# Kernel optimization log

Hardware: AMD Instinct MI355X
Metric: run time of the kernel (lower is better)

The kernel has to match this reference:

```python
import jax, jax.numpy as jnp
import numpy as np

N_NODES = 8192


def _gcn_norm(edge_index, num_nodes):
    # PyG GCNConv default: add self-loops, symmetric normalization.
    src, dst = edge_index[0], edge_index[1]
    loop = jnp.arange(num_nodes, dtype=src.dtype)
    src = jnp.concatenate([src, loop])
    dst = jnp.concatenate([dst, loop])
    deg = jax.ops.segment_sum(jnp.ones_like(dst, dtype=jnp.float32), dst,
                              num_segments=num_nodes)
    dis = jnp.where(deg > 0, jax.lax.rsqrt(jnp.maximum(deg, 1.0)), 0.0)
    norm = dis[src] * dis[dst]  # [E + N]
    return src, dst, norm


def _gcn_conv(x, W, b, src, dst, norm, num_nodes):
    h = x @ W                           # [N, F_out] dense GEMM
    msg = h[src] * norm[:, None]        # gather + scale, [E+N, F_out]
    out = jax.ops.segment_sum(msg, dst, num_segments=num_nodes)  # scatter-add
    return out + b


def setup_inputs() -> dict:
    key = jax.random.key(0)
    ks = jax.random.split(key, 8)
    N, E, F_in, H1, H2, F_out = N_NODES, 65536, 512, 4096, 1024, 10
    x = jax.random.normal(ks[0], (N, F_in), dtype=jnp.float32)
    edge_index = jax.random.randint(ks[1], (2, E), 0, N, dtype=jnp.int64)
    # Glorot-ish scaled weights
    W1 = jax.random.normal(ks[2], (F_in, H1), dtype=jnp.float32) * (1.0 / np.sqrt(F_in))
    b1 = jnp.zeros((H1,), dtype=jnp.float32)
    W2 = jax.random.normal(ks[3], (H1, H2), dtype=jnp.float32) * (1.0 / np.sqrt(H1))
    b2 = jnp.zeros((H2,), dtype=jnp.float32)
    W3 = jax.random.normal(ks[4], (H2, F_out), dtype=jnp.float32) * (1.0 / np.sqrt(H2))
    b3 = jnp.zeros((F_out,), dtype=jnp.float32)
    return {"x": x, "W1": W1, "b1": b1, "W2": W2, "b2": b2,
            "W3": W3, "b3": b3, "edge_index": edge_index}


def reference(x, W1, b1, W2, b2, W3, b3, edge_index):
    N = N_NODES
    src, dst, norm = _gcn_norm(edge_index, N)
    h = _gcn_conv(x.astype(jnp.float32), W1, b1, src, dst, norm, N)
    h = jax.nn.relu(h)  # dropout is identity in eval mode
    h = _gcn_conv(h, W2, b2, src, dst, norm, N)
    h = jax.nn.relu(h)
    h = _gcn_conv(h, W3, b3, src, dst, norm, N)
    return jax.nn.log_softmax(h, axis=1)
```

## Files before the change

kernel.cpp:

```cpp
#include <hip/hip_runtime.h>
#include <math.h>

#define N_NODES 8192
#define N_EDGES 65536
#define F_IN    512
#define HID1    4096
#define HID2    1024
#define F_OUT   10
#define H3_STRIDE 12

typedef __bf16 bf16x8 __attribute__((ext_vector_type(8)));
typedef float floatx4 __attribute__((ext_vector_type(4)));

static __device__ __forceinline__ unsigned short f2bf(float f) {
    union { float f; unsigned u; } v; v.f = f;
    unsigned r = v.u + 0x7fffu + ((v.u >> 16) & 1u);
    return (unsigned short)(r >> 16);
}
static __device__ __forceinline__ float bf2f(unsigned short u) {
    union { unsigned u; float f; } v; v.u = ((unsigned)u) << 16;
    return v.f;
}

__global__ void deg_kernel(const int* __restrict__ ei, int* __restrict__ deg) {
    int e = blockIdx.x * blockDim.x + threadIdx.x;
    if (e < N_EDGES) atomicAdd(&deg[ei[N_EDGES + e]], 1);
}

__global__ __launch_bounds__(1024) void scan_kernel(const int* __restrict__ deg,
                                                    int* __restrict__ row_ptr,
                                                    int* __restrict__ cnt) {
    __shared__ int sums[1024];
    int t = threadIdx.x;
    int base = t * 8;
    int local[8];
    int run = 0;
#pragma unroll
    for (int i = 0; i < 8; i++) { local[i] = run; run += deg[base + i]; cnt[base + i] = 0; }
    sums[t] = run;
    __syncthreads();
    for (int off = 1; off < 1024; off <<= 1) {
        int val = (t >= off) ? sums[t - off] : 0;
        __syncthreads();
        sums[t] += val;
        __syncthreads();
    }
    int offset = (t == 0) ? 0 : sums[t - 1];
#pragma unroll
    for (int i = 0; i < 8; i++) row_ptr[base + i] = offset + local[i];
    if (t == 1023) row_ptr[N_NODES] = sums[1023];
}

__global__ void fill_kernel(const int* __restrict__ ei, const int* __restrict__ deg,
                            const int* __restrict__ row_ptr, int* __restrict__ cnt,
                            int* __restrict__ csr_src, float* __restrict__ csr_w) {
    int e = blockIdx.x * blockDim.x + threadIdx.x;
    if (e < N_EDGES) {
        int s = ei[e];
        int d = ei[N_EDGES + e];
        int slot = row_ptr[d] + atomicAdd(&cnt[d], 1);
        csr_src[slot] = s;
        csr_w[slot] = rsqrtf((float)((deg[s] + 1) * (deg[d] + 1)));
    }
}

static __device__ __forceinline__ void transpose_body(
        const float* __restrict__ W, unsigned short* __restrict__ Wt,
        int K, int N, int k0, int n0, int tid, float (*t)[33]) {
    int c = tid & 31, r8 = tid >> 5;
#pragma unroll
    for (int i = 0; i < 4; i++) {
        int r = r8 + i * 8;
        t[r][c] = W[(size_t)(k0 + r) * N + n0 + c];
    }
    __syncthreads();
#pragma unroll
    for (int i = 0; i < 4; i++) {
        int r = r8 + i * 8;
        Wt[(size_t)(n0 + r) * K + k0 + c] = f2bf(t[c][r]);
    }
}

__global__ __launch_bounds__(256) void prep_kernel(
        const float* __restrict__ x, unsigned short* __restrict__ xb,
        const float* __restrict__ W1, unsigned short* __restrict__ W1t,
        const float* __restrict__ W2, unsigned short* __restrict__ W2t) {
    __shared__ float t[32][33];
    int b = blockIdx.x, tid = threadIdx.x;
    if (b < 4096) {
        int i = b * 256 + tid;
        float4 a = ((const float4*)x)[i];
        ushort4 o;
        o.x = f2bf(a.x); o.y = f2bf(a.y); o.z = f2bf(a.z); o.w = f2bf(a.w);
        ((ushort4*)xb)[i] = o;
    } else if (b < 6144) {
        int bb = b - 4096;
        transpose_body(W1, W1t, F_IN, HID1, (bb >> 7) * 32, (bb & 127) * 32, tid, t);
    } else {
        int bb = b - 6144;
        transpose_body(W2, W2t, HID1, HID2, (bb >> 5) * 32, (bb & 31) * 32, tid, t);
    }
}

__global__ __launch_bounds__(256) void agg1_kernel(
        const unsigned short* __restrict__ xb, const int* __restrict__ row_ptr,
        const int* __restrict__ csr_src, const float* __restrict__ csr_w,
        const int* __restrict__ deg, unsigned short* __restrict__ out) {
    int v = blockIdx.x * 2 + (threadIdx.x >> 7);
    int t = threadIdx.x & 127;
    const ushort4* x4 = (const ushort4*)xb;
    float sw = 1.0f / (float)(deg[v] + 1);
    ushort4 a = x4[(size_t)v * 128 + t];
    float ax = sw * bf2f(a.x), ay = sw * bf2f(a.y), az = sw * bf2f(a.z), aw = sw * bf2f(a.w);
    int e = row_ptr[v], end = row_ptr[v + 1];
    for (; e + 2 <= end; e += 2) {
        int s0 = csr_src[e], s1 = csr_src[e + 1];
        float w0 = csr_w[e], w1 = csr_w[e + 1];
        ushort4 b0 = x4[(size_t)s0 * 128 + t];
        ushort4 b1 = x4[(size_t)s1 * 128 + t];
        ax += w0 * bf2f(b0.x) + w1 * bf2f(b1.x);
        ay += w0 * bf2f(b0.y) + w1 * bf2f(b1.y);
        az += w0 * bf2f(b0.z) + w1 * bf2f(b1.z);
        aw += w0 * bf2f(b0.w) + w1 * bf2f(b1.w);
    }
    if (e < end) {
        int s = csr_src[e];
        float w = csr_w[e];
        ushort4 b = x4[(size_t)s * 128 + t];
        ax += w * bf2f(b.x); ay += w * bf2f(b.y); az += w * bf2f(b.z); aw += w * bf2f(b.w);
    }
    ushort4 o;
    o.x = f2bf(ax); o.y = f2bf(ay); o.z = f2bf(az); o.w = f2bf(aw);
    ((ushort4*)out)[(size_t)v * 128 + t] = o;
}

__global__ __launch_bounds__(256) void agg2_kernel(
        const unsigned short* __restrict__ h, const int* __restrict__ row_ptr,
        const int* __restrict__ csr_src, const float* __restrict__ csr_w,
        const int* __restrict__ deg, const float* __restrict__ bias,
        unsigned short* __restrict__ out) {
    int v = blockIdx.x;
    int t = threadIdx.x;
    const ushort4* h4 = (const ushort4*)h;
    float sw = 1.0f / (float)(deg[v] + 1);
    ushort4 a = h4[(size_t)v * 256 + t];
    float ax = sw * bf2f(a.x), ay = sw * bf2f(a.y), az = sw * bf2f(a.z), aw = sw * bf2f(a.w);
    int e = row_ptr[v], end = row_ptr[v + 1];
    for (; e + 2 <= end; e += 2) {
        int s0 = csr_src[e], s1 = csr_src[e + 1];
        float w0 = csr_w[e], w1 = csr_w[e + 1];
        ushort4 b0 = h4[(size_t)s0 * 256 + t];
        ushort4 b1 = h4[(size_t)s1 * 256 + t];
        ax += w0 * bf2f(b0.x) + w1 * bf2f(b1.x);
        ay += w0 * bf2f(b0.y) + w1 * bf2f(b1.y);
        az += w0 * bf2f(b0.z) + w1 * bf2f(b1.z);
        aw += w0 * bf2f(b0.w) + w1 * bf2f(b1.w);
    }
    if (e < end) {
        int s = csr_src[e];
        float w = csr_w[e];
        ushort4 b = h4[(size_t)s * 256 + t];
        ax += w * bf2f(b.x); ay += w * bf2f(b.y); az += w * bf2f(b.z); aw += w * bf2f(b.w);
    }
    float4 bb = ((const float4*)bias)[t];
    ushort4 o;
    o.x = f2bf(fmaxf(ax + bb.x, 0.0f)); o.y = f2bf(fmaxf(ay + bb.y, 0.0f));
    o.z = f2bf(fmaxf(az + bb.z, 0.0f)); o.w = f2bf(fmaxf(aw + bb.w, 0.0f));
    ((ushort4*)out)[(size_t)v * 256 + t] = o;
}

template <bool OUT_BF16, bool BIAS, bool RELU>
__global__ __launch_bounds__(256) void gemm_mfma_kernel(
        const unsigned short* __restrict__ A,
        const unsigned short* __restrict__ Bt,
        const float* __restrict__ bias,
        void* __restrict__ C,
        int M, int N, int K) {
    __shared__ unsigned short As[128 * 64];
    __shared__ unsigned short Bs[128 * 64];
    int tid = threadIdx.x;
    int wave = tid >> 6, lane = tid & 63;
    int wm = wave >> 1, wn = wave & 1;
    int GN = N >> 7;
    int b = blockIdx.x;
    int ntile = (b >> 3) % GN;
    int mtile = ((b >> 3) / GN) * 8 + (b & 7);
    int m0 = mtile * 128, n0 = ntile * 128;
    int lrow = lane & 15, lquad = lane >> 4;

    floatx4 acc[4][4] = {};

    for (int k0 = 0; k0 < K; k0 += 64) {
#pragma unroll
        for (int j = 0; j < 4; j++) {
            int idx = j * 256 + tid;
            int r = idx >> 3;
            int kc = (idx & 7) ^ (r & 7);
            __builtin_amdgcn_global_load_lds(
                (const __attribute__((address_space(1))) void*)(A + (size_t)(m0 + r) * K + k0 + kc * 8),
                (__attribute__((address_space(3))) void*)(&As[idx * 8]), 16, 0, 0);
            __builtin_amdgcn_global_load_lds(
                (const __attribute__((address_space(1))) void*)(Bt + (size_t)(n0 + r) * K + k0 + kc * 8),
                (__attribute__((address_space(3))) void*)(&Bs[idx * 8]), 16, 0, 0);
        }
        __syncthreads();
#pragma unroll
        for (int kk = 0; kk < 2; kk++) {
            bf16x8 af[4], bfr[4];
#pragma unroll
            for (int mt = 0; mt < 4; mt++) {
                int R = wm * 64 + mt * 16 + lrow;
                int c = kk * 4 + lquad;
                af[mt] = *(const bf16x8*)&As[(R * 8 + (c ^ (R & 7))) * 8];
            }
#pragma unroll
            for (int nt = 0; nt < 4; nt++) {
                int R = wn * 64 + nt * 16 + lrow;
                int c = kk * 4 + lquad;
                bfr[nt] = *(const bf16x8*)&Bs[(R * 8 + (c ^ (R & 7))) * 8];
            }
#pragma unroll
            for (int mt = 0; mt < 4; mt++)
#pragma unroll
                for (int nt = 0; nt < 4; nt++)
                    acc[mt][nt] = __builtin_amdgcn_mfma_f32_16x16x32_bf16(
                        af[mt], bfr[nt], acc[mt][nt], 0, 0, 0);
        }
        __syncthreads();
    }

#pragma unroll
    for (int mt = 0; mt < 4; mt++) {
#pragma unroll
        for (int nt = 0; nt < 4; nt++) {
            int col = n0 + wn * 64 + nt * 16 + lrow;
            float bv = BIAS ? bias[col] : 0.0f;
#pragma unroll
            for (int r = 0; r < 4; r++) {
                int row = m0 + wm * 64 + mt * 16 + lquad * 4 + r;
                float v = acc[mt][nt][r] + bv;
                if (RELU) v = fmaxf(v, 0.0f);
                if (OUT_BF16)
                    ((unsigned short*)C)[(size_t)row * N + col] = f2bf(v);
                else
                    ((float*)C)[(size_t)row * N + col] = v;
            }
        }
    }
}

__global__ __launch_bounds__(256) void gemm3_kernel(const unsigned short* __restrict__ A,
                                                    const float* __restrict__ W3,
                                                    float* __restrict__ H3) {
    __shared__ float w3s[HID2 * F_OUT];
    int tid = threadIdx.x;
    for (int i = tid; i < HID2 * F_OUT; i += 256) w3s[i] = W3[i];
    __syncthreads();
    int r = tid >> 3, sub = tid & 7;
    int row = blockIdx.x * 32 + r;
    const ushort4* a4p = (const ushort4*)A + (size_t)row * 256;
    float acc[F_OUT] = {};
#pragma unroll
    for (int i = 0; i < 32; i++) {
        ushort4 a = a4p[i * 8 + sub];
        int k = i * 32 + sub * 4;
        float a0 = bf2f(a.x), a1 = bf2f(a.y), a2 = bf2f(a.z), a3 = bf2f(a.w);
#pragma unroll
        for (int c = 0; c < F_OUT; c++)
            acc[c] += a0 * w3s[k * F_OUT + c] + a1 * w3s[(k + 1) * F_OUT + c] +
                      a2 * w3s[(k + 2) * F_OUT + c] + a3 * w3s[(k + 3) * F_OUT + c];
    }
#pragma unroll
    for (int c = 0; c < F_OUT; c++) {
        acc[c] += __shfl_xor(acc[c], 1, 64);
        acc[c] += __shfl_xor(acc[c], 2, 64);
        acc[c] += __shfl_xor(acc[c], 4, 64);
    }
    if (sub == 0) {
#pragma unroll
        for (int c = 0; c < F_OUT; c++) H3[row * H3_STRIDE + c] = acc[c];
    }
}

__global__ void final_kernel(const float* __restrict__ h3, const int* __restrict__ row_ptr,
                             const int* __restrict__ csr_src, const float* __restrict__ csr_w,
                             const int* __restrict__ deg, const float* __restrict__ b3,
                             float* __restrict__ out) {
    int v = blockIdx.x * blockDim.x + threadIdx.x;
    if (v >= N_NODES) return;
    const float4* h4 = (const float4*)h3;
    float sw = 1.0f / (float)(deg[v] + 1);
    float a[12];
    *(float4*)&a[0] = h4[v * 3];
    *(float4*)&a[4] = h4[v * 3 + 1];
    *(float4*)&a[8] = h4[v * 3 + 2];
    float acc[F_OUT];
#pragma unroll
    for (int c = 0; c < F_OUT; c++) acc[c] = b3[c] + sw * a[c];
    int end = row_ptr[v + 1];
    for (int e = row_ptr[v]; e < end; e++) {
        int s = csr_src[e];
        float w = csr_w[e];
        float bsrc[12];
        *(float4*)&bsrc[0] = h4[s * 3];
        *(float4*)&bsrc[4] = h4[s * 3 + 1];
        *(float4*)&bsrc[8] = h4[s * 3 + 2];
#pragma unroll
        for (int c = 0; c < F_OUT; c++) acc[c] += w * bsrc[c];
    }
    float m = acc[0];
#pragma unroll
    for (int c = 1; c < F_OUT; c++) m = fmaxf(m, acc[c]);
    float ssum = 0.0f;
#pragma unroll
    for (int c = 0; c < F_OUT; c++) ssum += expf(acc[c] - m);
    float l = logf(ssum);
#pragma unroll
    for (int c = 0; c < F_OUT; c++) out[v * F_OUT + c] = acc[c] - m - l;
}

extern "C" void kernel_launch(void* const* d_in, const int* in_sizes, int n_in,
                              void* d_out, int out_size, void* d_ws, size_t ws_size,
                              hipStream_t stream) {
    const float* x  = (const float*)d_in[0];
    const float* W1 = (const float*)d_in[1];
    const float* b1 = (const float*)d_in[2];
    const float* W2 = (const float*)d_in[3];
    const float* b2 = (const float*)d_in[4];
    const float* W3 = (const float*)d_in[5];
    const float* b3 = (const float*)d_in[6];
    const int*   ei = (const int*)d_in[7];
    float* out = (float*)d_out;

    char* p = (char*)d_ws;
    int*   deg     = (int*)p;    p += N_NODES * 4;
    int*   cnt     = (int*)p;    p += N_NODES * 4;
    int*   row_ptr = (int*)p;    p += 33024;
    int*   csr_src = (int*)p;    p += N_EDGES * 4;
    float* csr_w   = (float*)p;  p += N_EDGES * 4;
    float* h3      = (float*)p;  p += N_NODES * H3_STRIDE * 4;
    unsigned short* xb    = (unsigned short*)p; p += (size_t)N_NODES * F_IN * 2;
    unsigned short* agg_x = (unsigned short*)p; p += (size_t)N_NODES * F_IN * 2;
    unsigned short* W1t   = (unsigned short*)p; p += (size_t)HID1 * F_IN * 2;
    unsigned short* W2t   = (unsigned short*)p; p += (size_t)HID2 * HID1 * 2;
    unsigned short* h1    = (unsigned short*)p; p += (size_t)N_NODES * HID1 * 2;
    unsigned short* h2pre = (unsigned short*)p; p += (size_t)N_NODES * HID2 * 2;
    unsigned short* agg2b = (unsigned short*)p; p += (size_t)N_NODES * HID2 * 2;

    hipMemsetAsync(deg, 0, N_NODES * 4, stream);
    deg_kernel<<<N_EDGES / 256, 256, 0, stream>>>(ei, deg);
    scan_kernel<<<1, 1024, 0, stream>>>(deg, row_ptr, cnt);
    fill_kernel<<<N_EDGES / 256, 256, 0, stream>>>(ei, deg, row_ptr, cnt, csr_src, csr_w);

    prep_kernel<<<10240, 256, 0, stream>>>(x, xb, W1, W1t, W2, W2t);

    agg1_kernel<<<N_NODES / 2, 256, 0, stream>>>(xb, row_ptr, csr_src, csr_w, deg, agg_x);
    gemm_mfma_kernel<true, true, true><<<(HID1 / 128) * (N_NODES / 128), 256, 0, stream>>>(
        agg_x, W1t, b1, h1, N_NODES, HID1, F_IN);

    gemm_mfma_kernel<true, false, false><<<(HID2 / 128) * (N_NODES / 128), 256, 0, stream>>>(
        h1, W2t, nullptr, h2pre, N_NODES, HID2, HID1);
    agg2_kernel<<<N_NODES, 256, 0, stream>>>(h2pre, row_ptr, csr_src, csr_w, deg, b2, agg2b);

    gemm3_kernel<<<N_NODES / 32, 256, 0, stream>>>(agg2b, W3, h3);
    final_kernel<<<N_NODES / 256, 256, 0, stream>>>(h3, row_ptr, csr_src, csr_w, deg, b3, out);
}
```

Measured before the change: 301.1 us.

## Fuse degree histogram into scan and move third GEMM to MFMA

Merges the memset, the global-atomic degree kernel and the scan into a single one-block kernel that builds the histogram with shared-memory atomics, which removes two launches. The small 1024x10 final GEMM now runs on bf16 MFMA 16x16x32 with W3 transposed and padded to 16 columns in LDS, replacing a scalar FMA loop. H3 stride grows to 16 floats so the output tile can be written directly. The cost is a serial single-block histogram over all edges, and W3 is now rounded to bf16.

New measurement: 302.0 us. No clear change (+0.3%).

```diff
diff --git a/kernel.cpp b/kernel.cpp
--- a/kernel.cpp
+++ b/kernel.cpp
@@ -7,7 +7,8 @@
 #define HID1    4096
 #define HID2    1024
 #define F_OUT   10
-#define H3_STRIDE 12
+#define H3_STRIDE 16
+#define W3S_STRIDE 1032
 
 typedef __bf16 bf16x8 __attribute__((ext_vector_type(8)));
 typedef float floatx4 __attribute__((ext_vector_type(4)));
@@ -22,21 +23,30 @@
     return v.f;
 }
 
-__global__ void deg_kernel(const int* __restrict__ ei, int* __restrict__ deg) {
-    int e = blockIdx.x * blockDim.x + threadIdx.x;
-    if (e < N_EDGES) atomicAdd(&deg[ei[N_EDGES + e]], 1);
-}
-
-__global__ __launch_bounds__(1024) void scan_kernel(const int* __restrict__ deg,
-                                                    int* __restrict__ row_ptr,
-                                                    int* __restrict__ cnt) {
+__global__ __launch_bounds__(1024) void hist_scan_kernel(
+        const int* __restrict__ ei, int* __restrict__ deg,
+        int* __restrict__ row_ptr, int* __restrict__ cnt) {
+    __shared__ int hist[N_NODES];
     __shared__ int sums[1024];
     int t = threadIdx.x;
+#pragma unroll
+    for (int i = 0; i < 8; i++) hist[t + i * 1024] = 0;
+    __syncthreads();
+#pragma unroll
+    for (int i = 0; i < 64; i++) {
+        int d = ei[N_EDGES + i * 1024 + t];
+        atomicAdd(&hist[d], 1);
+    }
+    __syncthreads();
     int base = t * 8;
-    int local[8];
-    int run = 0;
-#pragma unroll
-    for (int i = 0; i < 8; i++) { local[i] = run; run += deg[base + i]; cnt[base + i] = 0; }
+    int local[8], run = 0;
+#pragma unroll
+    for (int i = 0; i < 8; i++) {
+        int dv = hist[base + i];
+        deg[base + i] = dv;
+        cnt[base + i] = 0;
+        local[i] = run; run += dv;
+    }
     sums[t] = run;
     __syncthreads();
     for (int off = 1; off < 1024; off <<= 1) {
@@ -249,37 +259,33 @@
     }
 }
 
-__global__ __launch_bounds__(256) void gemm3_kernel(const unsigned short* __restrict__ A,
-                                                    const float* __restrict__ W3,
-                                                    float* __restrict__ H3) {
-    __shared__ float w3s[HID2 * F_OUT];
+__global__ __launch_bounds__(256) void gemm3_mfma_kernel(
+        const unsigned short* __restrict__ A,
+        const float* __restrict__ W3,
+        float* __restrict__ H3) {
+    __shared__ unsigned short w3s[16 * W3S_STRIDE];
     int tid = threadIdx.x;
-    for (int i = tid; i < HID2 * F_OUT; i += 256) w3s[i] = W3[i];
-    __syncthreads();
-    int r = tid >> 3, sub = tid & 7;
-    int row = blockIdx.x * 32 + r;
-    const ushort4* a4p = (const ushort4*)A + (size_t)row * 256;
-    float acc[F_OUT] = {};
-#pragma unroll
-    for (int i = 0; i < 32; i++) {
-        ushort4 a = a4p[i * 8 + sub];
-        int k = i * 32 + sub * 4;
-        float a0 = bf2f(a.x), a1 = bf2f(a.y), a2 = bf2f(a.z), a3 = bf2f(a.w);
-#pragma unroll
-        for (int c = 0; c < F_OUT; c++)
-            acc[c] += a0 * w3s[k * F_OUT + c] + a1 * w3s[(k + 1) * F_OUT + c] +
-                      a2 * w3s[(k + 2) * F_OUT + c] + a3 * w3s[(k + 3) * F_OUT + c];
-    }
-#pragma unroll
-    for (int c = 0; c < F_OUT; c++) {
-        acc[c] += __shfl_xor(acc[c], 1, 64);
-        acc[c] += __shfl_xor(acc[c], 2, 64);
-        acc[c] += __shfl_xor(acc[c], 4, 64);
-    }
-    if (sub == 0) {
-#pragma unroll
-        for (int c = 0; c < F_OUT; c++) H3[row * H3_STRIDE + c] = acc[c];
-    }
+    for (int i = tid; i < 16 * W3S_STRIDE; i += 256) w3s[i] = 0;
+    __syncthreads();
+    for (int i = tid; i < HID2 * F_OUT; i += 256) {
+        int k = i / F_OUT, c = i % F_OUT;
+        w3s[c * W3S_STRIDE + k] = f2bf(W3[i]);
+    }
+    __syncthreads();
+    int wave = tid >> 6, lane = tid & 63;
+    int lrow = lane & 15, lquad = lane >> 4;
+    int m0 = (blockIdx.x * 4 + wave) * 16;
+    floatx4 acc = {};
+    const unsigned short* arow = A + (size_t)(m0 + lrow) * HID2 + lquad * 8;
+#pragma unroll
+    for (int kk = 0; kk < 32; kk++) {
+        bf16x8 af = *(const bf16x8*)(arow + kk * 32);
+        bf16x8 bf = *(const bf16x8*)&w3s[lrow * W3S_STRIDE + kk * 32 + lquad * 8];
+        acc = __builtin_amdgcn_mfma_f32_16x16x32_bf16(af, bf, acc, 0, 0, 0);
+    }
+#pragma unroll
+    for (int r = 0; r < 4; r++)
+        H3[(size_t)(m0 + lquad * 4 + r) * H3_STRIDE + lrow] = acc[r];
 }
 
 __global__ void final_kernel(const float* __restrict__ h3, const int* __restrict__ row_ptr,
@@ -291,9 +297,9 @@
     const float4* h4 = (const float4*)h3;
     float sw = 1.0f / (float)(deg[v] + 1);
     float a[12];
-    *(float4*)&a[0] = h4[v * 3];
-    *(float4*)&a[4] = h4[v * 3 + 1];
-    *(float4*)&a[8] = h4[v * 3 + 2];
+    *(float4*)&a[0] = h4[v * 4];
+    *(float4*)&a[4] = h4[v * 4 + 1];
+    *(float4*)&a[8] = h4[v * 4 + 2];
     float acc[F_OUT];
 #pragma unroll
     for (int c = 0; c < F_OUT; c++) acc[c] = b3[c] + sw * a[c];
@@ -302,9 +308,9 @@
         int s = csr_src[e];
         float w = csr_w[e];
         float bsrc[12];
-        *(float4*)&bsrc[0] = h4[s * 3];
-        *(float4*)&bsrc[4] = h4[s * 3 + 1];
-        *(float4*)&bsrc[8] = h4[s * 3 + 2];
+        *(float4*)&bsrc[0] = h4[s * 4];
+        *(float4*)&bsrc[4] = h4[s * 4 + 1];
+        *(float4*)&bsrc[8] = h4[s * 4 + 2];
 #pragma unroll
         for (int c = 0; c < F_OUT; c++) acc[c] += w * bsrc[c];
     }
@@ -347,9 +353,7 @@
     unsigned short* h2pre = (unsigned short*)p; p += (size_t)N_NODES * HID2 * 2;
     unsigned short* agg2b = (unsigned short*)p; p += (size_t)N_NODES * HID2 * 2;
 
-    hipMemsetAsync(deg, 0, N_NODES * 4, stream);
-    deg_kernel<<<N_EDGES / 256, 256, 0, stream>>>(ei, deg);
-    scan_kernel<<<1, 1024, 0, stream>>>(deg, row_ptr, cnt);
+    hist_scan_kernel<<<1, 1024, 0, stream>>>(ei, deg, row_ptr, cnt);
     fill_kernel<<<N_EDGES / 256, 256, 0, stream>>>(ei, deg, row_ptr, cnt, csr_src, csr_w);
 
     prep_kernel<<<10240, 256, 0, stream>>>(x, xb, W1, W1t, W2, W2t);
@@ -362,6 +366,6 @@
         h1, W2t, nullptr, h2pre, N_NODES, HID2, HID1);
     agg2_kernel<<<N_NODES, 256, 0, stream>>>(h2pre, row_ptr, csr_src, csr_w, deg, b2, agg2b);
 
-    gemm3_kernel<<<N_NODES / 32, 256, 0, stream>>>(agg2b, W3, h3);
+    gemm3_mfma_kernel<<<N_NODES / 64, 256, 0, stream>>>(agg2b, W3, h3);
     final_kernel<<<N_NODES / 256, 256, 0, stream>>>(h3, row_ptr, csr_src, csr_w, deg, b3, out);
 }
```
